# Optimization experiments

Measured on AMD Instinct MI355X. Metric: run time of the kernel, lower is better.

## Reference

```python
import jax, jax.numpy as jnp
import numpy as np

N = 4096      # number of nodes (tokens)
U = 128       # units (feature dim)
E = 131072    # number of edges (avg degree 32)


def _sage(x, src, dst, W_l, b_l, W_r):
    """PyG SAGEConv with mean aggregation.
    out = lin_l(mean_{j->i} x_j) + lin_r(x_i); lin_l has bias, lin_r does not.
    """
    n = x.shape[0]
    agg = jax.ops.segment_sum(x[src], dst, num_segments=n)
    deg = jax.ops.segment_sum(jnp.ones((src.shape[0],), x.dtype), dst, num_segments=n)
    agg = agg / jnp.maximum(deg, 1.0)[:, None]  # nodes w/o in-edges -> 0
    return agg @ W_l.T + b_l + x @ W_r.T


def setup_inputs() -> dict:
    key = jax.random.key(0)
    ks = jax.random.split(key, 20)
    s = 1.0 / np.sqrt(U)
    inp = {
        "x": jax.random.normal(ks[0], (N, U), jnp.float32),
        "edge_index": jax.random.randint(ks[1], (2, E), 0, N, jnp.int64),
        "batch": jnp.zeros((N,), jnp.int64),
        # conv_first
        "Wf_l": jax.random.normal(ks[2], (U, U), jnp.float32) * s,
        "bf_l": jnp.zeros((U,), jnp.float32),
        "Wf_r": jax.random.normal(ks[3], (U, U), jnp.float32) * s,
        # conv_common[0]
        "Wcm_l": jax.random.normal(ks[4], (U, U), jnp.float32) * s,
        "bcm_l": jnp.zeros((U,), jnp.float32),
        "Wcm_r": jax.random.normal(ks[5], (U, U), jnp.float32) * s,
        # conv_actor[0]
        "Wa_l": jax.random.normal(ks[6], (U, U), jnp.float32) * s,
        "ba_l": jnp.zeros((U,), jnp.float32),
        "Wa_r": jax.random.normal(ks[7], (U, U), jnp.float32) * s,
        # conv_critic[0]
        "Wcr_l": jax.random.normal(ks[8], (U, U), jnp.float32) * s,
        "bcr_l": jnp.zeros((U,), jnp.float32),
        "Wcr_r": jax.random.normal(ks[9], (U, U), jnp.float32) * s,
        # final_actor: Linear(2U, 1); final_critic: Linear(U, 1)
        "Wfa": jax.random.normal(ks[10], (1, 2 * U), jnp.float32) * (1.0 / np.sqrt(2 * U)),
        "bfa": jnp.zeros((1,), jnp.float32),
        "Wfc": jax.random.normal(ks[11], (1, U), jnp.float32) * s,
        "bfc": jnp.zeros((1,), jnp.float32),
    }
    return inp


def reference(x, edge_index, batch, Wf_l, bf_l, Wf_r, Wcm_l, bcm_l, Wcm_r,
              Wa_l, ba_l, Wa_r, Wcr_l, bcr_l, Wcr_r, Wfa, bfa, Wfc, bfc):
    src, dst = edge_index[0], edge_index[1]
    h = jnp.tanh(_sage(x, src, dst, Wf_l, bf_l, Wf_r))
    h = jnp.tanh(_sage(h, src, dst, Wcm_l, bcm_l, Wcm_r))

    # actor head: 1 SAGE layer (no activation since it is the last)
    x_actor = _sage(h, src, dst, Wa_l, ba_l, Wa_r)
    n = x_actor.shape[0]
    # pairwise row (i, j) feature = concat(x_actor[i], x_actor[j]) fed to Linear(2U,1).
    # Algebraically: score[i,j] = x_actor[i] @ w1 + x_actor[j] @ w2 + b  (same math,
    w1, w2 = Wfa[0, :U], Wfa[0, U:]
    scores = (x_actor @ w1)[:, None] + (x_actor @ w2)[None, :] + bfa[0]  # [N, N]
    edge_actor = jax.nn.log_softmax(scores.reshape(-1))[:, None]  # log_softmax over dim 0 of [N*N, 1]

    # critic head on detached features
    x_critic = _sage(jax.lax.stop_gradient(h), src, dst, Wcr_l, bcr_l, Wcr_r)
    cp = x_critic @ Wfc[0]  # [N]
    s = (cp[:, None] + cp[None, :]) * 0.5 + bfc[0]  # score[i,j] = ((c_i+c_j)/2) @ w + b
    edge_critic = jnp.tanh(jnp.mean(s)).reshape(1, 1)  # global_mean_pool over all N^2 rows
    return edge_actor, edge_critic
```

## Files before the change

kernel.cpp:

```cpp
#include <hip/hip_runtime.h>
#include <cstddef>

#define NN 4096
#define UF 128
#define NE 131072
#define SLOT_SHIFT 7
#define SLOTS (1 << SLOT_SHIFT)

typedef __attribute__((ext_vector_type(8))) short short8;
typedef __attribute__((ext_vector_type(4))) float f32x4;
typedef unsigned short bf16_t;

__device__ __forceinline__ short f2bf(float f) {
  unsigned u = __float_as_uint(f);
  unsigned r = (u + 0x7fffu + ((u >> 16) & 1u)) >> 16;
  return (short)r;
}
__device__ __forceinline__ float bf2f(unsigned short u) {
  return __uint_as_float(((unsigned)u) << 16);
}
__device__ __forceinline__ short8 cvt8(float4 w0, float4 w1) {
  short8 s;
  s[0] = f2bf(w0.x); s[1] = f2bf(w0.y); s[2] = f2bf(w0.z); s[3] = f2bf(w0.w);
  s[4] = f2bf(w1.x); s[5] = f2bf(w1.y); s[6] = f2bf(w1.z); s[7] = f2bf(w1.w);
  return s;
}

__device__ __forceinline__ int detect_is32(const void* ei) {
  const long long* e64 = (const long long*)ei;
  long long v = e64[threadIdx.x & 63];
  return (__ballot(v < 0 || v >= NN) != 0ull) ? 1 : 0;
}
__device__ __forceinline__ int edge_at(const void* ei, int is32, int idx) {
  if (is32) return ((const int*)ei)[idx];
  return (int)((const long long*)ei)[idx];
}

__device__ __forceinline__ float2 ld_row(const float* feat, int row, int lane) {
  return *((const float2*)(feat + (size_t)row * UF) + lane);
}
__device__ __forceinline__ float2 ld_row(const bf16_t* feat, int row, int lane) {
  ushort2 u = *((const ushort2*)(feat + (size_t)row * UF) + lane);
  float2 f; f.x = bf2f(u.x); f.y = bf2f(u.y); return f;
}
__device__ __forceinline__ short8 load_own(const float* feat, int row, int kk) {
  const float* src = feat + (size_t)row * UF + kk;
  float4 a0 = *(const float4*)src, a1 = *(const float4*)(src + 4);
  return cvt8(a0, a1);
}
__device__ __forceinline__ short8 load_own(const bf16_t* feat, int row, int kk) {
  return *(const short8*)(feat + (size_t)row * UF + kk);
}
__device__ __forceinline__ void store_out(float* p, size_t i, float v) { p[i] = v; }
__device__ __forceinline__ void store_out(bf16_t* p, size_t i, float v) {
  p[i] = (bf16_t)f2bf(v);
}

__global__ void k_scatter(const void* __restrict__ ei,
                          int* __restrict__ cnt, int* __restrict__ csr) {
  int is32 = detect_is32(ei);
  int e = blockIdx.x * blockDim.x + threadIdx.x;
  if (e >= NE) return;
  int s = edge_at(ei, is32, e);
  int d = edge_at(ei, is32, NE + e);
  int pos = atomicAdd(&cnt[d], 1);
  if (pos < SLOTS) csr[(d << SLOT_SHIFT) + pos] = s;
}

template<typename T>
__device__ __forceinline__ void gather2(
    int base, const T* __restrict__ feat,
    const int* __restrict__ cnt, const int* __restrict__ csr,
    float (*As32)[140]) {
  const int t = threadIdx.x;
  const int lane = t & 63, wv = t >> 6;
  int nodeA = base + wv, nodeB = base + wv + 8;
  int nA = min(cnt[nodeA], SLOTS), nB = min(cnt[nodeB], SLOTS);
  int sA = nodeA << SLOT_SHIFT, sB = nodeB << SLOT_SHIFT;
  float ax0 = 0.f, ax1 = 0.f, ay0 = 0.f, ay1 = 0.f;
  float bx0 = 0.f, bx1 = 0.f, by0 = 0.f, by1 = 0.f;
  int iters = (max(nA, nB) + 7) >> 3;
  for (int it = 0; it < iters; ++it) {
    int e0 = it * 8;
    int idx[16];
#pragma unroll
    for (int j = 0; j < 8; ++j) { int ee = e0 + j; idx[j]     = csr[sA + (ee < nA ? ee : 0)]; }
#pragma unroll
    for (int j = 0; j < 8; ++j) { int ee = e0 + j; idx[8 + j] = csr[sB + (ee < nB ? ee : 0)]; }
#pragma unroll
    for (int j = 0; j < 16; ++j) { unsigned u = (unsigned)idx[j]; idx[j] = (u < NN) ? (int)u : 0; }
    float2 v[16];
#pragma unroll
    for (int j = 0; j < 16; ++j) v[j] = ld_row(feat, idx[j], lane);
#pragma unroll
    for (int j = 0; j < 8; ++j) {
      bool ok = (e0 + j) < nA;
      if (j & 1) { ax1 += ok ? v[j].x : 0.f; ay1 += ok ? v[j].y : 0.f; }
      else       { ax0 += ok ? v[j].x : 0.f; ay0 += ok ? v[j].y : 0.f; }
    }
#pragma unroll
    for (int j = 0; j < 8; ++j) {
      bool ok = (e0 + j) < nB;
      if (j & 1) { bx1 += ok ? v[8+j].x : 0.f; by1 += ok ? v[8+j].y : 0.f; }
      else       { bx0 += ok ? v[8+j].x : 0.f; by0 += ok ? v[8+j].y : 0.f; }
    }
  }
  float invA = 1.0f / (float)max(nA, 1);
  float invB = 1.0f / (float)max(nB, 1);
  float2 rA; rA.x = (ax0 + ax1) * invA; rA.y = (ay0 + ay1) * invA;
  float2 rB; rB.x = (bx0 + bx1) * invB; rB.y = (by0 + by1) * invB;
  *(float2*)&As32[wv][2 * lane]     = rA;
  *(float2*)&As32[wv + 8][2 * lane] = rB;
}

template<bool TANH, typename TIN, typename TOUT>
__global__ __launch_bounds__(512, 2) void k_agglayer(
    const TIN* __restrict__ feat, const int* __restrict__ cnt,
    const int* __restrict__ csr,
    const float* __restrict__ Wl, const float* __restrict__ bl,
    const float* __restrict__ Wr, TOUT* __restrict__ out) {
  __shared__ float As32[16][140];
  const int t = threadIdx.x;
  const int base = blockIdx.x * 16;
  const int lane = t & 63, w = t >> 6;

  gather2(base, feat, cnt, csr, As32);
  __syncthreads();

  const int row = lane & 15;
  const int ks8 = (lane >> 4) * 8;
  const int o = w * 16 + row;
  f32x4 acc = {0.f, 0.f, 0.f, 0.f};
#pragma unroll
  for (int kc = 0; kc < 8; ++kc) {
    short8 a;
    if (kc < 4) {
      const float* pa = &As32[row][kc * 32 + ks8];
      float4 a0 = *(const float4*)pa, a1 = *(const float4*)(pa + 4);
      a = cvt8(a0, a1);
    } else {
      a = load_own(feat, base + row, (kc - 4) * 32 + ks8);
    }
    int kg = kc * 32 + ks8;
    const float* ws = (kg < 128) ? (Wl + (size_t)o * UF + kg)
                                 : (Wr + (size_t)o * UF + (kg - 128));
    float4 w0 = *(const float4*)ws, w1 = *(const float4*)(ws + 4);
    short8 b = cvt8(w0, w1);
    acc = __builtin_amdgcn_mfma_f32_16x16x32_bf16(a, b, acc, 0, 0, 0);
  }
  int rb = (lane >> 4) * 4;
  float bias = bl[o];
#pragma unroll
  for (int r = 0; r < 4; ++r) {
    float v = acc[r] + bias;
    if (TANH) v = tanhf(v);
    store_out(out, (size_t)(base + rb + r) * UF + o, v);
  }
}

__global__ __launch_bounds__(512, 2) void k_aggheads(
    const bf16_t* __restrict__ feat, const int* __restrict__ cnt,
    const int* __restrict__ csr,
    const float* __restrict__ Wa_l, const float* __restrict__ ba_l,
    const float* __restrict__ Wa_r,
    const float* __restrict__ Wcr_l, const float* __restrict__ bcr_l,
    const float* __restrict__ Wcr_r,
    const float* __restrict__ Wfa, const float* __restrict__ Wfc,
    float* __restrict__ a1, float* __restrict__ a2, float* __restrict__ sums) {
  __shared__ float As32[16][140];
  __shared__ float red[3][16][9];
  const int t = threadIdx.x;
  const int base = blockIdx.x * 16;
  const int lane = t & 63, w = t >> 6;

  gather2(base, feat, cnt, csr, As32);
  __syncthreads();

  const int row = lane & 15;
  const int ks8 = (lane >> 4) * 8;
  const int o = w * 16 + row;
  f32x4 accA = {0.f, 0.f, 0.f, 0.f};
  f32x4 accC = {0.f, 0.f, 0.f, 0.f};
#pragma unroll
  for (int kc = 0; kc < 8; ++kc) {
    short8 a;
    if (kc < 4) {
      const float* pa = &As32[row][kc * 32 + ks8];
      float4 a0 = *(const float4*)pa, a1v = *(const float4*)(pa + 4);
      a = cvt8(a0, a1v);
    } else {
      a = load_own(feat, base + row, (kc - 4) * 32 + ks8);
    }
    int kg = kc * 32 + ks8;
    const float* sA = (kg < 128) ? (Wa_l  + (size_t)o * UF + kg)
                                 : (Wa_r  + (size_t)o * UF + (kg - 128));
    const float* sC = (kg < 128) ? (Wcr_l + (size_t)o * UF + kg)
                                 : (Wcr_r + (size_t)o * UF + (kg - 128));
    float4 wa0 = *(const float4*)sA, wa1 = *(const float4*)(sA + 4);
    float4 wc0 = *(const float4*)sC, wc1 = *(const float4*)(sC + 4);
    short8 ba = cvt8(wa0, wa1);
    short8 bc = cvt8(wc0, wc1);
    accA = __builtin_amdgcn_mfma_f32_16x16x32_bf16(a, ba, accA, 0, 0, 0);
    accC = __builtin_amdgcn_mfma_f32_16x16x32_bf16(a, bc, accC, 0, 0, 0);
  }
  int col = lane & 15, rb = (lane >> 4) * 4;
  float baA = ba_l[o], baC = bcr_l[o];
  float w1 = Wfa[o], w2 = Wfa[UF + o], wfc = Wfc[o];
  float p1[4], p2[4], pc[4];
#pragma unroll
  for (int r = 0; r < 4; ++r) {
    float xa = accA[r] + baA;
    float xc = accC[r] + baC;
    p1[r] = xa * w1; p2[r] = xa * w2; pc[r] = xc * wfc;
  }
#pragma unroll
  for (int d = 1; d < 16; d <<= 1) {
#pragma unroll
    for (int r = 0; r < 4; ++r) {
      p1[r] += __shfl_xor(p1[r], d, 64);
      p2[r] += __shfl_xor(p2[r], d, 64);
      pc[r] += __shfl_xor(pc[r], d, 64);
    }
  }
  if (col == 0) {
#pragma unroll
    for (int r = 0; r < 4; ++r) {
      red[0][rb + r][w] = p1[r];
      red[1][rb + r][w] = p2[r];
      red[2][rb + r][w] = pc[r];
    }
  }
  __syncthreads();
  if (t < 48) {
    int q = t >> 4, n = t & 15;
    float s = 0.f;
#pragma unroll
    for (int j = 0; j < 8; ++j) s += red[q][n][j];
    if (q == 0) a1[base + n] = s;
    else if (q == 1) a2[base + n] = s;
    float v = (q < 2) ? expf(s) : s;
#pragma unroll
    for (int d = 1; d < 16; d <<= 1) v += __shfl_xor(v, d, 64);
    if ((t & 15) == 0) atomicAdd(&sums[q], v);
  }
}

__global__ __launch_bounds__(256) void k_write(
    const float* __restrict__ a1, const float* __restrict__ a2,
    const float* __restrict__ sums, const float* __restrict__ bfc,
    float* __restrict__ out) {
  const int t = blockIdx.x * 256 + threadIdx.x;
  const int lane = threadIdx.x & 63;
  float C = 0.f;
  if (lane == 0) C = -(logf(sums[0]) + logf(sums[1]));
  C = __shfl(C, 0, 64);
#pragma unroll
  for (int k = 0; k < 8; ++k) {
    int gid = t + k * 524288;
    int row = gid >> 10;
    int c = (gid & 1023) * 4;
    float Cr = C + a1[row];
    float4 v = *(const float4*)(a2 + c);
    float4 r; r.x = v.x + Cr; r.y = v.y + Cr; r.z = v.z + Cr; r.w = v.w + Cr;
    *(float4*)(out + (size_t)gid * 4) = r;
  }
  if (t == 0)
    out[(size_t)NN * NN] = tanhf(sums[2] * (1.0f / (float)NN) + bfc[0]);
}

extern "C" void kernel_launch(void* const* d_in, const int* in_sizes, int n_in,
                              void* d_out, int out_size, void* d_ws, size_t ws_size,
                              hipStream_t stream) {
  const float* x     = (const float*)d_in[0];
  const void*  ei    = d_in[1];
  const float* Wf_l  = (const float*)d_in[3];
  const float* bf_l  = (const float*)d_in[4];
  const float* Wf_r  = (const float*)d_in[5];
  const float* Wcm_l = (const float*)d_in[6];
  const float* bcm_l = (const float*)d_in[7];
  const float* Wcm_r = (const float*)d_in[8];
  const float* Wa_l  = (const float*)d_in[9];
  const float* ba_l  = (const float*)d_in[10];
  const float* Wa_r  = (const float*)d_in[11];
  const float* Wcr_l = (const float*)d_in[12];
  const float* bcr_l = (const float*)d_in[13];
  const float* Wcr_r = (const float*)d_in[14];
  const float* Wfa   = (const float*)d_in[15];
  const float* Wfc   = (const float*)d_in[17];
  const float* bfc   = (const float*)d_in[18];
  float* out = (float*)d_out;

  char* b = (char*)d_ws;
  size_t off = 0;
  float* sums = (float*)(b + off); off += 512;
  int* cnt = (int*)(b + off); off += (size_t)NN * 4;
  int* csr = (int*)(b + off); off += (size_t)NN * SLOTS * 4;
  float* a1 = (float*)(b + off); off += (size_t)NN * 4;
  float* a2 = (float*)(b + off); off += (size_t)NN * 4;
  bf16_t* h1 = (bf16_t*)(b + off); off += (size_t)NN * UF * 2;
  bf16_t* h2 = (bf16_t*)(b + off); off += (size_t)NN * UF * 2;
  if (ws_size < off) return;

  hipMemsetAsync(d_ws, 0, 512 + (size_t)NN * 4, stream);
  k_scatter<<<NE / 256, 256, 0, stream>>>(ei, cnt, csr);
  k_agglayer<true, float,  bf16_t><<<NN / 16, 512, 0, stream>>>(
      x,  cnt, csr, Wf_l,  bf_l,  Wf_r,  h1);
  k_agglayer<true, bf16_t, bf16_t><<<NN / 16, 512, 0, stream>>>(
      h1, cnt, csr, Wcm_l, bcm_l, Wcm_r, h2);
  k_aggheads<<<NN / 16, 512, 0, stream>>>(h2, cnt, csr, Wa_l, ba_l, Wa_r,
                                          Wcr_l, bcr_l, Wcr_r, Wfa, Wfc, a1, a2, sums);
  k_write<<<2048, 256, 0, stream>>>(a1, a2, sums, bfc, out);
}
```

Before: 86.35 us.

## Use 1024-thread blocks with one wave per node gather and split GEMM halves

Blocks grow from 512 to 1024 threads so each of 16 waves gathers one destination node instead of each wave handling two. The GEMM is split across waves: in the layer kernel half the waves do the aggregated (Wl) part and half the self (Wr) part, combined through shared memory, while the heads kernel gives actor and critic to separate wave groups. The intent is more memory-level parallelism in the latency-bound neighbour gather and less serial work per wave. The final output write now uses nontemporal stores to avoid polluting cache with the large N×N output. Costs are an extra barrier and shared buffer, plus possibly lower occupancy per CU with 1024-thread blocks.

New measurement: 85.19 us. Within noise of the previous version (-1.3%).

```diff
diff --git a/kernel.cpp b/kernel.cpp
--- a/kernel.cpp
+++ b/kernel.cpp
@@ -68,97 +68,93 @@
 }
 
 template<typename T>
-__device__ __forceinline__ void gather2(
-    int base, const T* __restrict__ feat,
+__device__ __forceinline__ void gather1(
+    int node, int lane, const T* __restrict__ feat,
     const int* __restrict__ cnt, const int* __restrict__ csr,
-    float (*As32)[140]) {
-  const int t = threadIdx.x;
-  const int lane = t & 63, wv = t >> 6;
-  int nodeA = base + wv, nodeB = base + wv + 8;
-  int nA = min(cnt[nodeA], SLOTS), nB = min(cnt[nodeB], SLOTS);
-  int sA = nodeA << SLOT_SHIFT, sB = nodeB << SLOT_SHIFT;
-  float ax0 = 0.f, ax1 = 0.f, ay0 = 0.f, ay1 = 0.f;
-  float bx0 = 0.f, bx1 = 0.f, by0 = 0.f, by1 = 0.f;
-  int iters = (max(nA, nB) + 7) >> 3;
+    float* __restrict__ dst) {
+  int n = min(cnt[node], SLOTS);
+  int s0 = node << SLOT_SHIFT;
+  float x0 = 0.f, x1 = 0.f, y0 = 0.f, y1 = 0.f;
+  int iters = (n + 15) >> 4;
   for (int it = 0; it < iters; ++it) {
-    int e0 = it * 8;
+    int e0 = it * 16;
     int idx[16];
 #pragma unroll
-    for (int j = 0; j < 8; ++j) { int ee = e0 + j; idx[j]     = csr[sA + (ee < nA ? ee : 0)]; }
-#pragma unroll
-    for (int j = 0; j < 8; ++j) { int ee = e0 + j; idx[8 + j] = csr[sB + (ee < nB ? ee : 0)]; }
+    for (int j = 0; j < 16; ++j) { int ee = e0 + j; idx[j] = csr[s0 + (ee < n ? ee : 0)]; }
 #pragma unroll
     for (int j = 0; j < 16; ++j) { unsigned u = (unsigned)idx[j]; idx[j] = (u < NN) ? (int)u : 0; }
     float2 v[16];
 #pragma unroll
     for (int j = 0; j < 16; ++j) v[j] = ld_row(feat, idx[j], lane);
 #pragma unroll
-    for (int j = 0; j < 8; ++j) {
-      bool ok = (e0 + j) < nA;
-      if (j & 1) { ax1 += ok ? v[j].x : 0.f; ay1 += ok ? v[j].y : 0.f; }
-      else       { ax0 += ok ? v[j].x : 0.f; ay0 += ok ? v[j].y : 0.f; }
-    }
-#pragma unroll
-    for (int j = 0; j < 8; ++j) {
-      bool ok = (e0 + j) < nB;
-      if (j & 1) { bx1 += ok ? v[8+j].x : 0.f; by1 += ok ? v[8+j].y : 0.f; }
-      else       { bx0 += ok ? v[8+j].x : 0.f; by0 += ok ? v[8+j].y : 0.f; }
-    }
-  }
-  float invA = 1.0f / (float)max(nA, 1);
-  float invB = 1.0f / (float)max(nB, 1);
-  float2 rA; rA.x = (ax0 + ax1) * invA; rA.y = (ay0 + ay1) * invA;
-  float2 rB; rB.x = (bx0 + bx1) * invB; rB.y = (by0 + by1) * invB;
-  *(float2*)&As32[wv][2 * lane]     = rA;
-  *(float2*)&As32[wv + 8][2 * lane] = rB;
+    for (int j = 0; j < 16; ++j) {
+      bool ok = (e0 + j) < n;
+      if (j & 1) { x1 += ok ? v[j].x : 0.f; y1 += ok ? v[j].y : 0.f; }
+      else       { x0 += ok ? v[j].x : 0.f; y0 += ok ? v[j].y : 0.f; }
+    }
+  }
+  float inv = 1.0f / (float)max(n, 1);
+  dst[2 * lane]     = (x0 + x1) * inv;
+  dst[2 * lane + 1] = (y0 + y1) * inv;
 }
 
 template<bool TANH, typename TIN, typename TOUT>
-__global__ __launch_bounds__(512, 2) void k_agglayer(
+__global__ __launch_bounds__(1024) void k_agglayer(
     const TIN* __restrict__ feat, const int* __restrict__ cnt,
     const int* __restrict__ csr,
     const float* __restrict__ Wl, const float* __restrict__ bl,
     const float* __restrict__ Wr, TOUT* __restrict__ out) {
   __shared__ float As32[16][140];
+  __shared__ float comb[8][64][4];
   const int t = threadIdx.x;
   const int base = blockIdx.x * 16;
   const int lane = t & 63, w = t >> 6;
-
-  gather2(base, feat, cnt, csr, As32);
-  __syncthreads();
-
   const int row = lane & 15;
   const int ks8 = (lane >> 4) * 8;
-  const int o = w * 16 + row;
+
+  gather1(base + w, lane, feat, cnt, csr, &As32[w][0]);
+  __syncthreads();
+
   f32x4 acc = {0.f, 0.f, 0.f, 0.f};
-#pragma unroll
-  for (int kc = 0; kc < 8; ++kc) {
-    short8 a;
-    if (kc < 4) {
+  if (w < 8) {
+    const int o = w * 16 + row;
+#pragma unroll
+    for (int kc = 0; kc < 4; ++kc) {
       const float* pa = &As32[row][kc * 32 + ks8];
       float4 a0 = *(const float4*)pa, a1 = *(const float4*)(pa + 4);
-      a = cvt8(a0, a1);
-    } else {
-      a = load_own(feat, base + row, (kc - 4) * 32 + ks8);
-    }
-    int kg = kc * 32 + ks8;
-    const float* ws = (kg < 128) ? (Wl + (size_t)o * UF + kg)
-                                 : (Wr + (size_t)o * UF + (kg - 128));
-    float4 w0 = *(const float4*)ws, w1 = *(const float4*)(ws + 4);
-    short8 b = cvt8(w0, w1);
-    acc = __builtin_amdgcn_mfma_f32_16x16x32_bf16(a, b, acc, 0, 0, 0);
-  }
-  int rb = (lane >> 4) * 4;
-  float bias = bl[o];
-#pragma unroll
-  for (int r = 0; r < 4; ++r) {
-    float v = acc[r] + bias;
-    if (TANH) v = tanhf(v);
-    store_out(out, (size_t)(base + rb + r) * UF + o, v);
-  }
-}
-
-__global__ __launch_bounds__(512, 2) void k_aggheads(
+      const float* ws = Wl + (size_t)o * UF + kc * 32 + ks8;
+      float4 w0 = *(const float4*)ws, w1 = *(const float4*)(ws + 4);
+      acc = __builtin_amdgcn_mfma_f32_16x16x32_bf16(cvt8(a0, a1), cvt8(w0, w1), acc, 0, 0, 0);
+    }
+  } else {
+    const int wt = w - 8;
+    const int o = wt * 16 + row;
+#pragma unroll
+    for (int kc = 0; kc < 4; ++kc) {
+      short8 a = load_own(feat, base + row, kc * 32 + ks8);
+      const float* ws = Wr + (size_t)o * UF + kc * 32 + ks8;
+      float4 w0 = *(const float4*)ws, w1 = *(const float4*)(ws + 4);
+      acc = __builtin_amdgcn_mfma_f32_16x16x32_bf16(a, cvt8(w0, w1), acc, 0, 0, 0);
+    }
+    *(f32x4*)&comb[wt][lane][0] = acc;
+  }
+  __syncthreads();
+
+  if (w < 8) {
+    const int o = w * 16 + row;
+    f32x4 other = *(const f32x4*)&comb[w][lane][0];
+    int rb = (lane >> 4) * 4;
+    float bias = bl[o];
+#pragma unroll
+    for (int r = 0; r < 4; ++r) {
+      float v = acc[r] + other[r] + bias;
+      if (TANH) v = tanhf(v);
+      store_out(out, (size_t)(base + rb + r) * UF + o, v);
+    }
+  }
+}
+
+__global__ __launch_bounds__(1024) void k_aggheads(
     const bf16_t* __restrict__ feat, const int* __restrict__ cnt,
     const int* __restrict__ csr,
     const float* __restrict__ Wa_l, const float* __restrict__ ba_l,
@@ -172,62 +168,71 @@
   const int t = threadIdx.x;
   const int base = blockIdx.x * 16;
   const int lane = t & 63, w = t >> 6;
-
-  gather2(base, feat, cnt, csr, As32);
-  __syncthreads();
-
   const int row = lane & 15;
   const int ks8 = (lane >> 4) * 8;
-  const int o = w * 16 + row;
-  f32x4 accA = {0.f, 0.f, 0.f, 0.f};
-  f32x4 accC = {0.f, 0.f, 0.f, 0.f};
-#pragma unroll
-  for (int kc = 0; kc < 8; ++kc) {
-    short8 a;
-    if (kc < 4) {
-      const float* pa = &As32[row][kc * 32 + ks8];
-      float4 a0 = *(const float4*)pa, a1v = *(const float4*)(pa + 4);
-      a = cvt8(a0, a1v);
-    } else {
-      a = load_own(feat, base + row, (kc - 4) * 32 + ks8);
-    }
-    int kg = kc * 32 + ks8;
-    const float* sA = (kg < 128) ? (Wa_l  + (size_t)o * UF + kg)
-                                 : (Wa_r  + (size_t)o * UF + (kg - 128));
-    const float* sC = (kg < 128) ? (Wcr_l + (size_t)o * UF + kg)
-                                 : (Wcr_r + (size_t)o * UF + (kg - 128));
-    float4 wa0 = *(const float4*)sA, wa1 = *(const float4*)(sA + 4);
-    float4 wc0 = *(const float4*)sC, wc1 = *(const float4*)(sC + 4);
-    short8 ba = cvt8(wa0, wa1);
-    short8 bc = cvt8(wc0, wc1);
-    accA = __builtin_amdgcn_mfma_f32_16x16x32_bf16(a, ba, accA, 0, 0, 0);
-    accC = __builtin_amdgcn_mfma_f32_16x16x32_bf16(a, bc, accC, 0, 0, 0);
-  }
+
+  gather1(base + w, lane, feat, cnt, csr, &As32[w][0]);
+  __syncthreads();
+
+  const int wt = w & 7;
+  const int o = wt * 16 + row;
+  const float* WL = (w < 8) ? Wa_l : Wcr_l;
+  const float* WR = (w < 8) ? Wa_r : Wcr_r;
+  f32x4 acc = {0.f, 0.f, 0.f, 0.f};
+#pragma unroll
+  for (int kc = 0; kc < 4; ++kc) {
+    const float* pa = &As32[row][kc * 32 + ks8];
+    float4 a0 = *(const float4*)pa, a1v = *(const float4*)(pa + 4);
+    const float* ws = WL + (size_t)o * UF + kc * 32 + ks8;
+    float4 w0 = *(const float4*)ws, w1 = *(const float4*)(ws + 4);
+    acc = __builtin_amdgcn_mfma_f32_16x16x32_bf16(cvt8(a0, a1v), cvt8(w0, w1), acc, 0, 0, 0);
+  }
+#pragma unroll
+  for (int kc = 0; kc < 4; ++kc) {
+    short8 a = load_own(feat, base + row, kc * 32 + ks8);
+    const float* ws = WR + (size_t)o * UF + kc * 32 + ks8;
+    float4 w0 = *(const float4*)ws, w1 = *(const float4*)(ws + 4);
+    acc = __builtin_amdgcn_mfma_f32_16x16x32_bf16(a, cvt8(w0, w1), acc, 0, 0, 0);
+  }
+
   int col = lane & 15, rb = (lane >> 4) * 4;
-  float baA = ba_l[o], baC = bcr_l[o];
-  float w1 = Wfa[o], w2 = Wfa[UF + o], wfc = Wfc[o];
-  float p1[4], p2[4], pc[4];
-#pragma unroll
-  for (int r = 0; r < 4; ++r) {
-    float xa = accA[r] + baA;
-    float xc = accC[r] + baC;
-    p1[r] = xa * w1; p2[r] = xa * w2; pc[r] = xc * wfc;
-  }
-#pragma unroll
-  for (int d = 1; d < 16; d <<= 1) {
+  if (w < 8) {
+    float baA = ba_l[o];
+    float w1f = Wfa[o], w2f = Wfa[UF + o];
+    float p1[4], p2[4];
 #pragma unroll
     for (int r = 0; r < 4; ++r) {
-      p1[r] += __shfl_xor(p1[r], d, 64);
-      p2[r] += __shfl_xor(p2[r], d, 64);
-      pc[r] += __shfl_xor(pc[r], d, 64);
-    }
-  }
-  if (col == 0) {
-#pragma unroll
-    for (int r = 0; r < 4; ++r) {
-      red[0][rb + r][w] = p1[r];
-      red[1][rb + r][w] = p2[r];
-      red[2][rb + r][w] = pc[r];
+      float xa = acc[r] + baA;
+      p1[r] = xa * w1f; p2[r] = xa * w2f;
+    }
+#pragma unroll
+    for (int d = 1; d < 16; d <<= 1) {
+#pragma unroll
+      for (int r = 0; r < 4; ++r) {
+        p1[r] += __shfl_xor(p1[r], d, 64);
+        p2[r] += __shfl_xor(p2[r], d, 64);
+      }
+    }
+    if (col == 0) {
+#pragma unroll
+      for (int r = 0; r < 4; ++r) {
+        red[0][rb + r][wt] = p1[r];
+        red[1][rb + r][wt] = p2[r];
+      }
+    }
+  } else {
+    float baC = bcr_l[o], wfc = Wfc[o];
+    float pc[4];
+#pragma unroll
+    for (int r = 0; r < 4; ++r) pc[r] = (acc[r] + baC) * wfc;
+#pragma unroll
+    for (int d = 1; d < 16; d <<= 1) {
+#pragma unroll
+      for (int r = 0; r < 4; ++r) pc[r] += __shfl_xor(pc[r], d, 64);
+    }
+    if (col == 0) {
+#pragma unroll
+      for (int r = 0; r < 4; ++r) red[2][rb + r][wt] = pc[r];
     }
   }
   __syncthreads();
@@ -261,8 +266,8 @@
     int c = (gid & 1023) * 4;
     float Cr = C + a1[row];
     float4 v = *(const float4*)(a2 + c);
-    float4 r; r.x = v.x + Cr; r.y = v.y + Cr; r.z = v.z + Cr; r.w = v.w + Cr;
-    *(float4*)(out + (size_t)gid * 4) = r;
+    f32x4 r; r[0] = v.x + Cr; r[1] = v.y + Cr; r[2] = v.z + Cr; r[3] = v.w + Cr;
+    __builtin_nontemporal_store(r, (f32x4*)(out + (size_t)gid * 4));
   }
   if (t == 0)
     out[(size_t)NN * NN] = tanhf(sums[2] * (1.0f / (float)NN) + bfc[0]);
@@ -301,13 +306,13 @@
   bf16_t* h2 = (bf16_t*)(b + off); off += (size_t)NN * UF * 2;
   if (ws_size < off) return;
 
-  hipMemsetAsync(d_ws, 0, 512 + (size_t)NN * 4, stream);
+  (void)hipMemsetAsync(d_ws, 0, 512 + (size_t)NN * 4, stream);
   k_scatter<<<NE / 256, 256, 0, stream>>>(ei, cnt, csr);
-  k_agglayer<true, float,  bf16_t><<<NN / 16, 512, 0, stream>>>(
+  k_agglayer<true, float,  bf16_t><<<NN / 16, 1024, 0, stream>>>(
       x,  cnt, csr, Wf_l,  bf_l,  Wf_r,  h1);
-  k_agglayer<true, bf16_t, bf16_t><<<NN / 16, 512, 0, stream>>>(
+  k_agglayer<true, bf16_t, bf16_t><<<NN / 16, 1024, 0, stream>>>(
       h1, cnt, csr, Wcm_l, bcm_l, Wcm_r, h2);
-  k_aggheads<<<NN / 16, 512, 0, stream>>>(h2, cnt, csr, Wa_l, ba_l, Wa_r,
-                                          Wcr_l, bcr_l, Wcr_r, Wfa, Wfc, a1, a2, sums);
+  k_aggheads<<<NN / 16, 1024, 0, stream>>>(h2, cnt, csr, Wa_l, ba_l, Wa_r,
+                                           Wcr_l, bcr_l, Wcr_r, Wfa, Wfc, a1, a2, sums);
   k_write<<<2048, 256, 0, stream>>>(a1, a2, sums, bfc, out);
 }
```
